# Optimization experiments

Hardware: AMD Instinct MI355X
Metric: run time of the kernel (lower is better)

The kernel has to match this reference:

```python
import jax, jax.numpy as jnp
import numpy as np
import math

IN_C, OUT_C, K, STYLE_DIM = 512, 512, 3, 512
EPS = 1e-8
SCALE = 1.0 / math.sqrt(IN_C * K * K)


def setup_inputs() -> dict:
    key = jax.random.key(0)
    k1, k2, k3, k4, k5 = jax.random.split(key, 5)
    x = jax.random.normal(k1, (8, IN_C, 64, 64), dtype=jnp.float32)
    style = jax.random.normal(k2, (8, STYLE_DIM), dtype=jnp.float32)
    weight = jax.random.normal(k3, (1, OUT_C, IN_C, K, K), dtype=jnp.float32)
    # nn.Linear(style_dim, in_channels): weight [in_channels, style_dim], bias [in_channels]
    lim = 1.0 / math.sqrt(STYLE_DIM)
    style_w = jax.random.uniform(k4, (IN_C, STYLE_DIM), dtype=jnp.float32, minval=-lim, maxval=lim)
    style_b = jax.random.uniform(k5, (IN_C,), dtype=jnp.float32, minval=-lim, maxval=lim)
    return {"x": x, "style": style, "weight": weight, "style_w": style_w, "style_b": style_b}


def _conv_one(xi, wi):
    # xi: [C,H,W], wi: [O,I,K,K]
    out = jax.lax.conv_general_dilated(
        xi[None], wi, window_strides=(1, 1), padding="SAME",
        dimension_numbers=("NCHW", "OIHW", "NCHW"))
    return out[0]


def reference(x, style, weight, style_w, style_b):
    N = x.shape[0]
    s = style @ style_w.T + style_b                      # [N, C_in]
    w = weight * SCALE                                    # [1,O,I,K,K]
    w = w * s[:, None, :, None, None]                     # [N,O,I,K,K]
    demod = jax.lax.rsqrt(jnp.sum(w * w, axis=(2, 3, 4)) + EPS)  # [N,O]
    w = w * demod[:, :, None, None, None]
    out = jax.vmap(_conv_one)(x, w)                       # [N,O,H,W]
    return out
```

## Files before the change

kernel.cpp:

```cpp
#include <hip/hip_runtime.h>
#include <stdint.h>

typedef unsigned short u16;
typedef __bf16 bf16x8 __attribute__((ext_vector_type(8)));
typedef float f32x4 __attribute__((ext_vector_type(4)));

#define SCALE_F 0.014731391274719742f

#define S_OFF   0u
#define DM_OFF  16384u
#define WSQ_OFF 32768u
#define WM_OFF  1081344u
#define XS_OFF  38830080u
#define WS_NEED 74514432u

__device__ __forceinline__ u16 f2bf(float f) {
  union { float f; uint32_t u; } c; c.f = f;
  return (u16)((c.u + 0x7FFFu + ((c.u >> 16) & 1u)) >> 16);
}

__device__ __forceinline__ void gload16(const void* g, void* l) {
  __builtin_amdgcn_global_load_lds(
      (const __attribute__((address_space(1))) uint32_t*)g,
      (__attribute__((address_space(3))) uint32_t*)l, 16, 0, 0);
}

__global__ void k_style(const float* __restrict__ style, const float* __restrict__ sw,
                        const float* __restrict__ sb, float* __restrict__ s) {
  int t = blockIdx.x * 256 + threadIdx.x;
  int n = t >> 9, c = t & 511;
  const float4* wr = (const float4*)(sw + (size_t)c * 512);
  const float4* st = (const float4*)(style + (size_t)n * 512);
  float acc = 0.f;
  #pragma unroll 4
  for (int d = 0; d < 128; ++d) {
    float4 a = st[d], b = wr[d];
    acc += a.x * b.x + a.y * b.y + a.z * b.z + a.w * b.w;
  }
  s[t] = acc + sb[c];
}

__global__ void k_wsq(const float* __restrict__ w, float* __restrict__ wsq) {
  int t = blockIdx.x * 256 + threadIdx.x;
  const float* p = w + (size_t)t * 9;
  float a = 0.f;
  #pragma unroll
  for (int r = 0; r < 9; ++r) a += p[r] * p[r];
  wsq[t] = a;
}

__global__ void k_demod(const float* __restrict__ s, const float* __restrict__ wsq,
                        float* __restrict__ dm) {
  int t = blockIdx.x * 256 + threadIdx.x;
  int n = t >> 9, o = t & 511;
  const float4* sp = (const float4*)(s + (size_t)n * 512);
  const float4* wp = (const float4*)(wsq + (size_t)o * 512);
  float acc = 0.f;
  #pragma unroll 4
  for (int d = 0; d < 128; ++d) {
    float4 a = sp[d], b = wp[d];
    acc += a.x * a.x * b.x + a.y * a.y * b.y + a.z * a.z * b.z + a.w * a.w * b.w;
  }
  dm[t] = rsqrtf((1.0f / 4608.0f) * acc + 1e-8f);
}

__global__ __launch_bounds__(256) void k_wmod2(
    const float* __restrict__ w, const float* __restrict__ s,
    const float* __restrict__ dm, u16* __restrict__ wm) {
  __shared__ float wlds[4608];
  __shared__ float slds[4096];
  const uint32_t o = blockIdx.x, t = threadIdx.x;
  #pragma unroll
  for (uint32_t c = 0; c < 18u; ++c)
    wlds[c * 256u + t] = w[(size_t)o * 4608u + c * 256u + t] * SCALE_F;
  #pragma unroll
  for (uint32_t c = 0; c < 16u; ++c)
    slds[c * 256u + t] = s[c * 256u + t];
  float dmv[8];
  #pragma unroll
  for (uint32_t nn = 0; nn < 8u; ++nn) dmv[nn] = dm[nn * 512u + o];
  __syncthreads();
  #pragma unroll 2
  for (uint32_t c = 0; c < 18u; ++c) {
    uint32_t idx = c * 256u + t;
    uint32_t i = idx & 511u, r = idx >> 9;
    float wv = wlds[i * 9u + r];
    #pragma unroll
    for (uint32_t nn = 0; nn < 8u; ++nn)
      wm[((size_t)nn * 512u + o) * 4608u + idx] = f2bf(wv * slds[nn * 512u + i] * dmv[nn]);
  }
}

__global__ void k_zero(uint4* __restrict__ p) {
  uint32_t t = blockIdx.x * 256u + threadIdx.x;
  uint4 z = {0u, 0u, 0u, 0u};
  p[t] = z;
}

__global__ __launch_bounds__(256) void k_xpose(const float* __restrict__ x,
                                               u16* __restrict__ xs) {
  __shared__ u16 tile[64][520];
  uint32_t b = blockIdx.x, n = b >> 6, hs = b & 63u;
  uint32_t t = threadIdx.x;
  const float* xr = x + ((size_t)n * 512u * 64u + hs) * 64u;
  #pragma unroll 4
  for (uint32_t p = 0; p < 32u; ++p) {
    uint32_t idx = p * 256u + t;
    uint32_t i = idx >> 4, w4 = (idx & 15u) * 4u;
    float4 v = *(const float4*)(xr + (size_t)i * 4096u + w4);
    tile[w4 + 0u][i] = f2bf(v.x);
    tile[w4 + 1u][i] = f2bf(v.y);
    tile[w4 + 2u][i] = f2bf(v.z);
    tile[w4 + 3u][i] = f2bf(v.w);
  }
  __syncthreads();
  u16* orow = xs + (((size_t)n * 66u + hs + 1u) * 66u + 1u) * 512u;
  #pragma unroll 4
  for (uint32_t p = 0; p < 16u; ++p) {
    uint32_t idx = p * 256u + t;
    uint32_t w = idx >> 6, i8 = (idx & 63u) * 8u;
    *(bf16x8*)(orow + (size_t)w * 512u + i8) = *(const bf16x8*)(&tile[w][i8]);
  }
}

__global__ __launch_bounds__(512, 2) void k_conv8(
    const u16* __restrict__ Wm, const u16* __restrict__ Xs, float* __restrict__ out)
{
  extern __shared__ u16 smem[];
  u16* As = smem;
  u16* Bs = smem + 32768;

  const uint32_t bid = blockIdx.x;
  const uint32_t swz = (bid & 7u) * 32u + (bid >> 3);
  const uint32_t n = swz >> 5, ot = (swz >> 4) & 1u, pt = swz & 15u;

  const uint32_t tid = threadIdx.x;
  const uint32_t wid = tid >> 6, lane = tid & 63u;
  const uint32_t l16 = lane & 15u, lg = lane >> 4;
  const uint32_t wm = wid >> 2, wn = wid & 3u;

  const u16* wmn = Wm + (size_t)n * 512u * 4608u;
  const u16* xsn = Xs + (size_t)n * 66u * 66u * 512u;

  f32x4 acc[8][4];
  f32x4 zero = {0.f, 0.f, 0.f, 0.f};
  #pragma unroll
  for (int m = 0; m < 8; ++m)
    #pragma unroll
    for (int nn = 0; nn < 4; ++nn) acc[m][nn] = zero;

  auto stage = [&](uint32_t h) {
    if (h >= 288u) return;
    const uint32_t Tt = h >> 2, q = h & 3u;
    const uint32_t buf = Tt & 1u;
    const uint32_t r = Tt >> 3, i0 = (Tt & 7u) << 6;
    const uint32_t kh = r / 3u, kw = r % 3u;
    const uint32_t half = q & 1u;
    #pragma unroll
    for (uint32_t j = 0; j < 2u; ++j) {
      const uint32_t sl = tid + j * 512u;
      const uint32_t row = sl >> 3, cl = sl & 7u;
      const uint32_t csrc = cl ^ (row & 7u);
      u16* dst;
      const u16* src;
      if (q < 2u) {
        const uint32_t R = half * 128u + row;
        const uint32_t hp = pt * 4u + (R >> 6) + kh, wp = (R & 63u) + kw;
        src = xsn + ((size_t)hp * 66u + wp) * 512u + i0 + csrc * 8u;
        dst = As + buf * 16384u + half * 8192u + (wid * 64u + j * 512u) * 8u;
      } else {
        const uint32_t o = ot * 256u + half * 128u + row;
        src = wmn + (size_t)o * 4608u + r * 512u + i0 + csrc * 8u;
        dst = Bs + buf * 16384u + half * 8192u + (wid * 64u + j * 512u) * 8u;
      }
      gload16(src, dst);
    }
  };

  for (uint32_t h = 0; h < 7u; ++h) stage(h);
  asm volatile("s_waitcnt vmcnt(6)" ::: "memory");
  __builtin_amdgcn_s_barrier();

  bf16x8 a[8][2], b01[2][2], b23[2][2];

  for (uint32_t T = 0; T < 72u; ++T) {
    const uint32_t buf = T & 1u;
    const u16* Ab = As + buf * 16384u;
    const u16* Bb = Bs + buf * 16384u;
    const uint32_t P = T * 4u;

    #pragma unroll
    for (uint32_t m = 0; m < 8u; ++m) {
      const uint32_t row = wm * 128u + m * 16u + l16;
      #pragma unroll
      for (uint32_t k = 0; k < 2u; ++k) {
        const uint32_t c = (k * 4u + lg) ^ (row & 7u);
        a[m][k] = *(const bf16x8*)(Ab + row * 64u + c * 8u);
      }
    }
    #pragma unroll
    for (uint32_t nn = 0; nn < 2u; ++nn) {
      const uint32_t row = wn * 64u + nn * 16u + l16;
      #pragma unroll
      for (uint32_t k = 0; k < 2u; ++k) {
        const uint32_t c = (k * 4u + lg) ^ (row & 7u);
        b01[nn][k] = *(const bf16x8*)(Bb + row * 64u + c * 8u);
      }
    }
    stage(P + 7u);
    __builtin_amdgcn_s_barrier();
    asm volatile("s_waitcnt lgkmcnt(0)" ::: "memory");
    __builtin_amdgcn_sched_barrier(0);
    __builtin_amdgcn_s_setprio(1);
    #pragma unroll
    for (uint32_t m = 0; m < 4u; ++m)
      #pragma unroll
      for (uint32_t nn = 0; nn < 2u; ++nn)
        #pragma unroll
        for (uint32_t k = 0; k < 2u; ++k)
          acc[m][nn] = __builtin_amdgcn_mfma_f32_16x16x32_bf16(a[m][k], b01[nn][k], acc[m][nn], 0, 0, 0);
    __builtin_amdgcn_s_setprio(0);
    __builtin_amdgcn_s_barrier();

    #pragma unroll
    for (uint32_t nn = 0; nn < 2u; ++nn) {
      const uint32_t row = wn * 64u + (nn + 2u) * 16u + l16;
      #pragma unroll
      for (uint32_t k = 0; k < 2u; ++k) {
        const uint32_t c = (k * 4u + lg) ^ (row & 7u);
        b23[nn][k] = *(const bf16x8*)(Bb + row * 64u + c * 8u);
      }
    }
    stage(P + 8u);
    __builtin_amdgcn_s_barrier();
    asm volatile("s_waitcnt lgkmcnt(0)" ::: "memory");
    __builtin_amdgcn_sched_barrier(0);
    __builtin_amdgcn_s_setprio(1);
    #pragma unroll
    for (uint32_t m = 0; m < 4u; ++m)
      #pragma unroll
      for (uint32_t nn = 0; nn < 2u; ++nn)
        #pragma unroll
        for (uint32_t k = 0; k < 2u; ++k)
          acc[m + 4u][nn] = __builtin_amdgcn_mfma_f32_16x16x32_bf16(a[m + 4u][k], b01[nn][k], acc[m + 4u][nn], 0, 0, 0);
    __builtin_amdgcn_s_setprio(0);
    __builtin_amdgcn_s_barrier();

    stage(P + 9u);
    __builtin_amdgcn_s_barrier();
    __builtin_amdgcn_s_setprio(1);
    #pragma unroll
    for (uint32_t m = 0; m < 4u; ++m)
      #pragma unroll
      for (uint32_t nn = 0; nn < 2u; ++nn)
        #pragma unroll
        for (uint32_t k = 0; k < 2u; ++k)
          acc[m][nn + 2u] = __builtin_amdgcn_mfma_f32_16x16x32_bf16(a[m][k], b23[nn][k], acc[m][nn + 2u], 0, 0, 0);
    __builtin_amdgcn_s_setprio(0);
    __builtin_amdgcn_s_barrier();

    stage(P + 10u);
    __builtin_amdgcn_s_barrier();
    __builtin_amdgcn_s_setprio(1);
    #pragma unroll
    for (uint32_t m = 0; m < 4u; ++m)
      #pragma unroll
      for (uint32_t nn = 0; nn < 2u; ++nn)
        #pragma unroll
        for (uint32_t k = 0; k < 2u; ++k)
          acc[m + 4u][nn + 2u] = __builtin_amdgcn_mfma_f32_16x16x32_bf16(a[m + 4u][k], b23[nn][k], acc[m + 4u][nn + 2u], 0, 0, 0);
    __builtin_amdgcn_s_setprio(0);
    if (T < 70u) {
      asm volatile("s_waitcnt vmcnt(6)" ::: "memory");
    } else if (T == 70u) {
      asm volatile("s_waitcnt vmcnt(0)" ::: "memory");
    }
    __builtin_amdgcn_s_barrier();
  }

  float* op = out + ((size_t)n * 512u + ot * 256u + wn * 64u) * 4096u + pt * 256u + wm * 128u;
  #pragma unroll
  for (uint32_t m = 0; m < 8u; ++m)
    #pragma unroll
    for (uint32_t nn = 0; nn < 4u; ++nn)
      *(f32x4*)(op + (size_t)(nn * 16u + l16) * 4096u + m * 16u + lg * 4u) = acc[m][nn];
}

extern "C" void kernel_launch(void* const* d_in, const int* in_sizes, int n_in,
                              void* d_out, int out_size, void* d_ws, size_t ws_size,
                              hipStream_t stream) {
  const float* x       = (const float*)d_in[0];
  const float* style   = (const float*)d_in[1];
  const float* weight  = (const float*)d_in[2];
  const float* style_w = (const float*)d_in[3];
  const float* style_b = (const float*)d_in[4];
  float* out = (float*)d_out;

  if (ws_size < (size_t)WS_NEED) return;

  char* ws = (char*)d_ws;
  float* s   = (float*)(ws + S_OFF);
  float* dm  = (float*)(ws + DM_OFF);
  float* wsq = (float*)(ws + WSQ_OFF);
  u16*   wm  = (u16*)(ws + WM_OFF);
  u16*   xs  = (u16*)(ws + XS_OFF);

  (void)hipFuncSetAttribute((const void*)k_conv8,
                            hipFuncAttributeMaxDynamicSharedMemorySize, 131072);

  hipLaunchKernelGGL(k_style, dim3(16),    dim3(256), 0, stream, style, style_w, style_b, s);
  hipLaunchKernelGGL(k_wsq,   dim3(1024),  dim3(256), 0, stream, weight, wsq);
  hipLaunchKernelGGL(k_demod, dim3(16),    dim3(256), 0, stream, s, wsq, dm);
  hipLaunchKernelGGL(k_wmod2, dim3(512),   dim3(256), 0, stream, weight, s, dm, wm);
  hipLaunchKernelGGL(k_zero,  dim3(8712),  dim3(256), 0, stream, (uint4*)xs);
  hipLaunchKernelGGL(k_xpose, dim3(512),   dim3(256), 0, stream, x, xs);
  hipLaunchKernelGGL(k_conv8, dim3(256),   dim3(512), 131072, stream, wm, xs, out);
}
```

Measured before the change: 328.3 us.

## Fuse demod into weight modulation, zero only borders, restructure transpose and conv staging

The separate wsq and demod kernels are folded into the weight-modulation kernel, which now computes demodulation per output channel with a block reduction. The full zeroing of the padded input buffer is replaced by a kernel that writes only the one-pixel border. The transpose kernel now loads eight channels per thread and writes packed 16-byte LDS stores. The conv main loop changes its prefetch schedule: B for the next tile and A two tiles ahead are staged separately, and the A fragment loads are split across sub-phases. The intent is fewer launches, less memory traffic and better load/MFMA interleaving. The risk is a shallower prefetch for B and changed vmcnt accounting.

Measured after the change: 301.5 us. 1.09x faster.

```diff
diff --git a/kernel.cpp b/kernel.cpp
--- a/kernel.cpp
+++ b/kernel.cpp
@@ -8,8 +8,6 @@
 #define SCALE_F 0.014731391274719742f
 
 #define S_OFF   0u
-#define DM_OFF  16384u
-#define WSQ_OFF 32768u
 #define WM_OFF  1081344u
 #define XS_OFF  38830080u
 #define WS_NEED 74514432u
@@ -40,82 +38,101 @@
   s[t] = acc + sb[c];
 }
 
-__global__ void k_wsq(const float* __restrict__ w, float* __restrict__ wsq) {
-  int t = blockIdx.x * 256 + threadIdx.x;
-  const float* p = w + (size_t)t * 9;
-  float a = 0.f;
-  #pragma unroll
-  for (int r = 0; r < 9; ++r) a += p[r] * p[r];
-  wsq[t] = a;
-}
-
-__global__ void k_demod(const float* __restrict__ s, const float* __restrict__ wsq,
-                        float* __restrict__ dm) {
-  int t = blockIdx.x * 256 + threadIdx.x;
-  int n = t >> 9, o = t & 511;
-  const float4* sp = (const float4*)(s + (size_t)n * 512);
-  const float4* wp = (const float4*)(wsq + (size_t)o * 512);
-  float acc = 0.f;
-  #pragma unroll 4
-  for (int d = 0; d < 128; ++d) {
-    float4 a = sp[d], b = wp[d];
-    acc += a.x * a.x * b.x + a.y * a.y * b.y + a.z * a.z * b.z + a.w * a.w * b.w;
-  }
-  dm[t] = rsqrtf((1.0f / 4608.0f) * acc + 1e-8f);
-}
-
-__global__ __launch_bounds__(256) void k_wmod2(
-    const float* __restrict__ w, const float* __restrict__ s,
-    const float* __restrict__ dm, u16* __restrict__ wm) {
+__global__ __launch_bounds__(256) void k_wmod3(
+    const float* __restrict__ w, const float* __restrict__ s, u16* __restrict__ wm) {
   __shared__ float wlds[4608];
   __shared__ float slds[4096];
+  __shared__ float red[8][4];
+  __shared__ float dmv_sh[8];
   const uint32_t o = blockIdx.x, t = threadIdx.x;
+  const uint32_t lane = t & 63u, wv = t >> 6;
   #pragma unroll
   for (uint32_t c = 0; c < 18u; ++c)
     wlds[c * 256u + t] = w[(size_t)o * 4608u + c * 256u + t] * SCALE_F;
   #pragma unroll
   for (uint32_t c = 0; c < 16u; ++c)
     slds[c * 256u + t] = s[c * 256u + t];
+  __syncthreads();
+  float part[8] = {0.f, 0.f, 0.f, 0.f, 0.f, 0.f, 0.f, 0.f};
+  #pragma unroll
+  for (uint32_t hh = 0; hh < 2u; ++hh) {
+    uint32_t i = hh * 256u + t;
+    float q = 0.f;
+    #pragma unroll
+    for (uint32_t r = 0; r < 9u; ++r) { float a = wlds[i * 9u + r]; q += a * a; }
+    #pragma unroll
+    for (uint32_t nn = 0; nn < 8u; ++nn) {
+      float sv = slds[nn * 512u + i];
+      part[nn] += q * sv * sv;
+    }
+  }
+  #pragma unroll
+  for (uint32_t nn = 0; nn < 8u; ++nn) {
+    float v = part[nn];
+    #pragma unroll
+    for (uint32_t off = 32u; off >= 1u; off >>= 1) v += __shfl_down(v, off);
+    if (lane == 0u) red[nn][wv] = v;
+  }
+  __syncthreads();
+  if (t < 8u)
+    dmv_sh[t] = rsqrtf(red[t][0] + red[t][1] + red[t][2] + red[t][3] + 1e-8f);
+  __syncthreads();
   float dmv[8];
   #pragma unroll
-  for (uint32_t nn = 0; nn < 8u; ++nn) dmv[nn] = dm[nn * 512u + o];
-  __syncthreads();
+  for (uint32_t nn = 0; nn < 8u; ++nn) dmv[nn] = dmv_sh[nn];
   #pragma unroll 2
   for (uint32_t c = 0; c < 18u; ++c) {
     uint32_t idx = c * 256u + t;
     uint32_t i = idx & 511u, r = idx >> 9;
-    float wv = wlds[i * 9u + r];
+    float wvv = wlds[i * 9u + r];
     #pragma unroll
     for (uint32_t nn = 0; nn < 8u; ++nn)
-      wm[((size_t)nn * 512u + o) * 4608u + idx] = f2bf(wv * slds[nn * 512u + i] * dmv[nn]);
-  }
-}
-
-__global__ void k_zero(uint4* __restrict__ p) {
-  uint32_t t = blockIdx.x * 256u + threadIdx.x;
+      wm[((size_t)nn * 512u + o) * 4608u + idx] = f2bf(wvv * slds[nn * 512u + i] * dmv[nn]);
+  }
+}
+
+__global__ void k_border(u16* __restrict__ xs) {
+  uint32_t tg = blockIdx.x * 256u + threadIdx.x;
+  uint32_t q = tg >> 6;
+  uint32_t r = tg & 63u;
+  uint32_t n = q / 260u, b = q % 260u;
+  uint32_t h, w;
+  if (b < 66u)        { h = 0u;  w = b; }
+  else if (b < 132u)  { h = 65u; w = b - 66u; }
+  else { uint32_t c = b - 132u; h = 1u + (c >> 1); w = (c & 1u) * 65u; }
   uint4 z = {0u, 0u, 0u, 0u};
-  p[t] = z;
+  *(uint4*)(xs + (((size_t)n * 66u + h) * 66u + w) * 512u + r * 8u) = z;
 }
 
 __global__ __launch_bounds__(256) void k_xpose(const float* __restrict__ x,
                                                u16* __restrict__ xs) {
-  __shared__ u16 tile[64][520];
+  __shared__ u16 tile[64][512];
   uint32_t b = blockIdx.x, n = b >> 6, hs = b & 63u;
   uint32_t t = threadIdx.x;
   const float* xr = x + ((size_t)n * 512u * 64u + hs) * 64u;
-  #pragma unroll 4
-  for (uint32_t p = 0; p < 32u; ++p) {
-    uint32_t idx = p * 256u + t;
-    uint32_t i = idx >> 4, w4 = (idx & 15u) * 4u;
-    float4 v = *(const float4*)(xr + (size_t)i * 4096u + w4);
-    tile[w4 + 0u][i] = f2bf(v.x);
-    tile[w4 + 1u][i] = f2bf(v.y);
-    tile[w4 + 2u][i] = f2bf(v.z);
-    tile[w4 + 3u][i] = f2bf(v.w);
+  uint32_t w4 = (t & 15u) * 4u;
+  uint32_t ib = (t >> 4) * 8u;
+  #pragma unroll
+  for (uint32_t p = 0; p < 4u; ++p) {
+    uint32_t i0 = p * 128u + ib;
+    float4 v[8];
+    #pragma unroll
+    for (uint32_t j = 0; j < 8u; ++j)
+      v[j] = *(const float4*)(xr + (size_t)(i0 + j) * 4096u + w4);
+    #pragma unroll
+    for (uint32_t k = 0; k < 4u; ++k) {
+      union { u16 h[8]; uint4 q; } pk;
+      #pragma unroll
+      for (uint32_t j = 0; j < 8u; ++j) {
+        float f = (k == 0u) ? v[j].x : (k == 1u) ? v[j].y : (k == 2u) ? v[j].z : v[j].w;
+        pk.h[j] = f2bf(f);
+      }
+      *(uint4*)&tile[w4 + k][i0] = pk.q;
+    }
   }
   __syncthreads();
   u16* orow = xs + (((size_t)n * 66u + hs + 1u) * 66u + 1u) * 512u;
-  #pragma unroll 4
+  #pragma unroll
   for (uint32_t p = 0; p < 16u; ++p) {
     uint32_t idx = p * 256u + t;
     uint32_t w = idx >> 6, i8 = (idx & 63u) * 8u;
@@ -149,36 +166,40 @@
     #pragma unroll
     for (int nn = 0; nn < 4; ++nn) acc[m][nn] = zero;
 
-  auto stage = [&](uint32_t h) {
-    if (h >= 288u) return;
-    const uint32_t Tt = h >> 2, q = h & 3u;
+  auto stageA = [&](uint32_t Tt, uint32_t half) {
+    if (Tt >= 72u) return;
     const uint32_t buf = Tt & 1u;
     const uint32_t r = Tt >> 3, i0 = (Tt & 7u) << 6;
     const uint32_t kh = r / 3u, kw = r % 3u;
-    const uint32_t half = q & 1u;
     #pragma unroll
     for (uint32_t j = 0; j < 2u; ++j) {
       const uint32_t sl = tid + j * 512u;
       const uint32_t row = sl >> 3, cl = sl & 7u;
       const uint32_t csrc = cl ^ (row & 7u);
-      u16* dst;
-      const u16* src;
-      if (q < 2u) {
-        const uint32_t R = half * 128u + row;
-        const uint32_t hp = pt * 4u + (R >> 6) + kh, wp = (R & 63u) + kw;
-        src = xsn + ((size_t)hp * 66u + wp) * 512u + i0 + csrc * 8u;
-        dst = As + buf * 16384u + half * 8192u + (wid * 64u + j * 512u) * 8u;
-      } else {
-        const uint32_t o = ot * 256u + half * 128u + row;
-        src = wmn + (size_t)o * 4608u + r * 512u + i0 + csrc * 8u;
-        dst = Bs + buf * 16384u + half * 8192u + (wid * 64u + j * 512u) * 8u;
-      }
-      gload16(src, dst);
+      const uint32_t R = half * 128u + row;
+      const uint32_t hp = pt * 4u + (R >> 6) + kh, wp = (R & 63u) + kw;
+      gload16(xsn + ((size_t)hp * 66u + wp) * 512u + i0 + csrc * 8u,
+              As + buf * 16384u + half * 8192u + (wid * 64u + j * 512u) * 8u);
     }
   };
-
-  for (uint32_t h = 0; h < 7u; ++h) stage(h);
-  asm volatile("s_waitcnt vmcnt(6)" ::: "memory");
+  auto stageB = [&](uint32_t Tt, uint32_t half) {
+    if (Tt >= 72u) return;
+    const uint32_t buf = Tt & 1u;
+    const uint32_t r = Tt >> 3, i0 = (Tt & 7u) << 6;
+    #pragma unroll
+    for (uint32_t j = 0; j < 2u; ++j) {
+      const uint32_t sl = tid + j * 512u;
+      const uint32_t row = sl >> 3, cl = sl & 7u;
+      const uint32_t csrc = cl ^ (row & 7u);
+      const uint32_t o = ot * 256u + half * 128u + row;
+      gload16(wmn + (size_t)o * 4608u + r * 512u + i0 + csrc * 8u,
+              Bs + buf * 16384u + half * 8192u + (wid * 64u + j * 512u) * 8u);
+    }
+  };
+
+  stageA(0u, 0u); stageA(0u, 1u); stageB(0u, 0u); stageB(0u, 1u);
+  stageA(1u, 0u); stageA(1u, 1u);
+  asm volatile("s_waitcnt vmcnt(4)" ::: "memory");
   __builtin_amdgcn_s_barrier();
 
   bf16x8 a[8][2], b01[2][2], b23[2][2];
@@ -187,10 +208,9 @@
     const uint32_t buf = T & 1u;
     const u16* Ab = As + buf * 16384u;
     const u16* Bb = Bs + buf * 16384u;
-    const uint32_t P = T * 4u;
-
-    #pragma unroll
-    for (uint32_t m = 0; m < 8u; ++m) {
+
+    #pragma unroll
+    for (uint32_t m = 0; m < 4u; ++m) {
       const uint32_t row = wm * 128u + m * 16u + l16;
       #pragma unroll
       for (uint32_t k = 0; k < 2u; ++k) {
@@ -207,7 +227,7 @@
         b01[nn][k] = *(const bf16x8*)(Bb + row * 64u + c * 8u);
       }
     }
-    stage(P + 7u);
+    stageB(T + 1u, 0u);
     __builtin_amdgcn_s_barrier();
     asm volatile("s_waitcnt lgkmcnt(0)" ::: "memory");
     __builtin_amdgcn_sched_barrier(0);
@@ -223,15 +243,15 @@
     __builtin_amdgcn_s_barrier();
 
     #pragma unroll
-    for (uint32_t nn = 0; nn < 2u; ++nn) {
-      const uint32_t row = wn * 64u + (nn + 2u) * 16u + l16;
+    for (uint32_t m = 0; m < 4u; ++m) {
+      const uint32_t row = wm * 128u + (m + 4u) * 16u + l16;
       #pragma unroll
       for (uint32_t k = 0; k < 2u; ++k) {
         const uint32_t c = (k * 4u + lg) ^ (row & 7u);
-        b23[nn][k] = *(const bf16x8*)(Bb + row * 64u + c * 8u);
-      }
-    }
-    stage(P + 8u);
+        a[m + 4u][k] = *(const bf16x8*)(Ab + row * 64u + c * 8u);
+      }
+    }
+    stageB(T + 1u, 1u);
     __builtin_amdgcn_s_barrier();
     asm volatile("s_waitcnt lgkmcnt(0)" ::: "memory");
     __builtin_amdgcn_sched_barrier(0);
@@ -246,8 +266,19 @@
     __builtin_amdgcn_s_setprio(0);
     __builtin_amdgcn_s_barrier();
 
-    stage(P + 9u);
-    __builtin_amdgcn_s_barrier();
+    #pragma unroll
+    for (uint32_t nn = 0; nn < 2u; ++nn) {
+      const uint32_t row = wn * 64u + (nn + 2u) * 16u + l16;
+      #pragma unroll
+      for (uint32_t k = 0; k < 2u; ++k) {
+        const uint32_t c = (k * 4u + lg) ^ (row & 7u);
+        b23[nn][k] = *(const bf16x8*)(Bb + row * 64u + c * 8u);
+      }
+    }
+    stageA(T + 2u, 0u);
+    __builtin_amdgcn_s_barrier();
+    asm volatile("s_waitcnt lgkmcnt(0)" ::: "memory");
+    __builtin_amdgcn_sched_barrier(0);
     __builtin_amdgcn_s_setprio(1);
     #pragma unroll
     for (uint32_t m = 0; m < 4u; ++m)
@@ -259,7 +290,7 @@
     __builtin_amdgcn_s_setprio(0);
     __builtin_amdgcn_s_barrier();
 
-    stage(P + 10u);
+    stageA(T + 2u, 1u);
     __builtin_amdgcn_s_barrier();
     __builtin_amdgcn_s_setprio(1);
     #pragma unroll
@@ -271,8 +302,8 @@
           acc[m + 4u][nn + 2u] = __builtin_amdgcn_mfma_f32_16x16x32_bf16(a[m + 4u][k], b23[nn][k], acc[m + 4u][nn + 2u], 0, 0, 0);
     __builtin_amdgcn_s_setprio(0);
     if (T < 70u) {
-      asm volatile("s_waitcnt vmcnt(6)" ::: "memory");
-    } else if (T == 70u) {
+      asm volatile("s_waitcnt vmcnt(4)" ::: "memory");
+    } else {
       asm volatile("s_waitcnt vmcnt(0)" ::: "memory");
     }
     __builtin_amdgcn_s_barrier();
@@ -299,20 +330,16 @@
   if (ws_size < (size_t)WS_NEED) return;
 
   char* ws = (char*)d_ws;
-  float* s   = (float*)(ws + S_OFF);
-  float* dm  = (float*)(ws + DM_OFF);
-  float* wsq = (float*)(ws + WSQ_OFF);
-  u16*   wm  = (u16*)(ws + WM_OFF);
-  u16*   xs  = (u16*)(ws + XS_OFF);
+  float* s  = (float*)(ws + S_OFF);
+  u16*   wm = (u16*)(ws + WM_OFF);
+  u16*   xs = (u16*)(ws + XS_OFF);
 
   (void)hipFuncSetAttribute((const void*)k_conv8,
                             hipFuncAttributeMaxDynamicSharedMemorySize, 131072);
 
-  hipLaunchKernelGGL(k_style, dim3(16),    dim3(256), 0, stream, style, style_w, style_b, s);
-  hipLaunchKernelGGL(k_wsq,   dim3(1024),  dim3(256), 0, stream, weight, wsq);
-  hipLaunchKernelGGL(k_demod, dim3(16),    dim3(256), 0, stream, s, wsq, dm);
-  hipLaunchKernelGGL(k_wmod2, dim3(512),   dim3(256), 0, stream, weight, s, dm, wm);
-  hipLaunchKernelGGL(k_zero,  dim3(8712),  dim3(256), 0, stream, (uint4*)xs);
-  hipLaunchKernelGGL(k_xpose, dim3(512),   dim3(256), 0, stream, x, xs);
-  hipLaunchKernelGGL(k_conv8, dim3(256),   dim3(512), 131072, stream, wm, xs, out);
-}
+  hipLaunchKernelGGL(k_style,  dim3(16),   dim3(256), 0, stream, style, style_w, style_b, s);
+  hipLaunchKernelGGL(k_wmod3,  dim3(512),  dim3(256), 0, stream, weight, s, wm);
+  hipLaunchKernelGGL(k_border, dim3(520),  dim3(256), 0, stream, xs);
+  hipLaunchKernelGGL(k_xpose,  dim3(512),  dim3(256), 0, stream, x, xs);
+  hipLaunchKernelGGL(k_conv8,  dim3(256),  dim3(512), 131072, stream, wm, xs, out);
+}
```
